# Optimization experiments

Hardware: AMD Instinct MI355X
Metric: run time of the kernel (lower is better)

The kernel has to match this reference:

```python
import jax, jax.numpy as jnp
import numpy as np

QB = 127.0  # act_bits=8 -> 2**(8-1)-1
EPS = 1e-5


def _ste(x, q):
    # straight-through estimator: forward = q, backward = identity
    return x + jax.lax.stop_gradient(q - x)


def bitlinear(x, W, b):
    """BitNet-b1.58 linear: ternary weights (per-tensor mean-abs scale),
    8-bit per-token absmax activations, dequantized matmul + bias."""
    w_scale = jnp.clip(jnp.mean(jnp.abs(W)), EPS, None)
    Wq = _ste(W, jnp.clip(jnp.round(W / w_scale), -1.0, 1.0) * w_scale)  # ternary * scale
    x_scale = jnp.clip(jnp.max(jnp.abs(x), axis=-1, keepdims=True), EPS, None)
    xq = _ste(x, jnp.clip(jnp.round(x * (QB / x_scale)), -QB - 1.0, QB) * (x_scale / QB))
    # x: [B, N, d_in], W: [d_out, d_in] -> [B, N, d_out]
    return jnp.einsum('bnd,hd->bnh', xq, Wq) + b


def setup_inputs() -> dict:
    key = jax.random.key(0)
    k0, k1, k2 = jax.random.split(key, 3)
    B, N, D = 8, 4096, 1024
    H = int(D * 4.0)
    x = jax.random.normal(k0, (B, N, D), dtype=jnp.float32)
    W1 = jax.random.normal(k1, (H, D), dtype=jnp.float32) * 0.02
    b1 = jnp.zeros((H,), dtype=jnp.float32)
    W2 = jax.random.normal(k2, (D, H), dtype=jnp.float32) * 0.02
    b2 = jnp.zeros((D,), dtype=jnp.float32)
    return {"x": x, "W1": W1, "b1": b1, "W2": W2, "b2": b2}


def reference(x, W1, b1, W2, b2):
    h = bitlinear(x, W1, b1)                 # [B, N, H]
    h = jax.nn.gelu(h, approximate=False)    # torch nn.GELU default = exact erf
    # dropout with p=0.0 is identity
    return bitlinear(h, W2, b2)              # [B, N, D]
```

## Files before the change

kernel.cpp:

```cpp
#include <hip/hip_runtime.h>
#include <hip/hip_bf16.h>
#include <math.h>


typedef int int32x4 __attribute__((ext_vector_type(4)));

typedef const void __attribute__((address_space(1))) gv_t;
typedef void __attribute__((address_space(3))) lv_t;

__device__ __forceinline__ void gload_lds16(const signed char* g,
                                            signed char* l) {
  __builtin_amdgcn_global_load_lds((gv_t*)g, (lv_t*)l, 16, 0, 0);
}

__device__ __forceinline__ float gelu_erf(float v) {
  return 0.5f * v * (1.0f + erff(v * 0.70710678118654752440f));
}

__device__ __forceinline__ void store_gt(float* p, float v) { *p = v; }
__device__ __forceinline__ void store_gt(__hip_bfloat16* p, float v) {
  unsigned u = __float_as_uint(v);
  u += 0x7fffu + ((u >> 16) & 1u);
  *(unsigned short*)p = (unsigned short)(u >> 16);
}

__device__ __forceinline__ void load4v(const float* p, float v[4]) {
  const float4 t = *(const float4*)p;
  v[0] = t.x; v[1] = t.y; v[2] = t.z; v[3] = t.w;
}
__device__ __forceinline__ void load4v(const __hip_bfloat16* p, float v[4]) {
  const ushort4 t = *(const ushort4*)p;
  v[0] = __uint_as_float((unsigned)t.x << 16);
  v[1] = __uint_as_float((unsigned)t.y << 16);
  v[2] = __uint_as_float((unsigned)t.z << 16);
  v[3] = __uint_as_float((unsigned)t.w << 16);
}

__global__ __launch_bounds__(256) void absmean_partial(
    const float* __restrict__ W, double* __restrict__ part) {
  const int tid = threadIdx.x;
  const long base = (long)blockIdx.x * 8192;
  double s = 0.0;
#pragma unroll
  for (int c = 0; c < 8; ++c) {
    const float4 v = *(const float4*)&W[base + c * 1024 + tid * 4];
    s += (double)fabsf(v.x) + (double)fabsf(v.y) +
         (double)fabsf(v.z) + (double)fabsf(v.w);
  }
  __shared__ double sm[256];
  sm[tid] = s; __syncthreads();
  for (int off = 128; off; off >>= 1) {
    if (tid < off) sm[tid] += sm[tid + off];
    __syncthreads();
  }
  if (tid == 0) part[blockIdx.x] = sm[0];
}

__global__ __launch_bounds__(256) void absmean_final(
    const double* __restrict__ part, double* __restrict__ out, double n) {
  const int tid = threadIdx.x;
  __shared__ double sm[256];
  sm[tid] = part[tid] + part[tid + 256];
  __syncthreads();
  for (int off = 128; off; off >>= 1) {
    if (tid < off) sm[tid] += sm[tid + off];
    __syncthreads();
  }
  if (tid == 0) out[0] = fmax(sm[0] / n, 1e-5);
}

__global__ __launch_bounds__(256) void quant_w(
    const float* __restrict__ W, const double* __restrict__ wsP,
    signed char* __restrict__ Wq) {
  const double ws = *wsP;
  const long i = ((long)blockIdx.x * 256 + threadIdx.x) * 4;
  const float4 v = *(const float4*)&W[i];
  const float vv[4] = {v.x, v.y, v.z, v.w};
  int pack = 0;
#pragma unroll
  for (int q = 0; q < 4; ++q) {
    double r = rint((double)vv[q] / ws);
    r = fmin(fmax(r, -1.0), 1.0);
    pack |= (((int)r) & 0xff) << (8 * q);
  }
  *(int*)&Wq[i] = pack;
}

template <int L, bool GELU, typename GT>
__global__ __launch_bounds__(256) void quant_rows(
    const GT* __restrict__ X, signed char* __restrict__ Xq,
    float* __restrict__ dsc) {
  constexpr int CH = L / 1024;
  const long row = blockIdx.x;
  const int tid = threadIdx.x;
  const GT* xr = X + row * (long)L;
  float v[CH][4];
  float m = 0.f;
#pragma unroll
  for (int c = 0; c < CH; ++c) {
    load4v(xr + c * 1024 + tid * 4, v[c]);
#pragma unroll
    for (int q = 0; q < 4; ++q) {
      if (GELU) v[c][q] = gelu_erf(v[c][q]);
      m = fmaxf(m, fabsf(v[c][q]));
    }
  }
#pragma unroll
  for (int off = 32; off; off >>= 1) m = fmaxf(m, __shfl_down(m, off, 64));
  __shared__ float wmx[4];
  if ((tid & 63) == 0) wmx[tid >> 6] = m;
  __syncthreads();
  float ms = fmaxf(fmaxf(wmx[0], wmx[1]), fmaxf(wmx[2], wmx[3]));
  ms = fmaxf(ms, 1e-5f);
  const double inv = 127.0 / (double)ms;
#pragma unroll
  for (int c = 0; c < CH; ++c) {
    int pack = 0;
#pragma unroll
    for (int q = 0; q < 4; ++q) {
      double r = rint((double)v[c][q] * inv);
      r = fmin(fmax(r, -128.0), 127.0);
      pack |= (((int)r) & 0xff) << (8 * q);
    }
    *(int*)&Xq[row * (long)L + c * 1024 + tid * 4] = pack;
  }
  if (tid == 0) dsc[row] = (float)((double)ms / 127.0);
}

template <typename GT>
__global__ __launch_bounds__(256, 2) void gemm_i8_occ(
    const signed char* __restrict__ A, const signed char* __restrict__ Bm,
    const float* __restrict__ dA, const double* __restrict__ wsB,
    const float* __restrict__ bias, GT* __restrict__ C,
    int K, int Ncol, int nx) {
  __shared__ signed char LDS[65536];
  const int tid = threadIdx.x;
  const int lane = tid & 63;
  const int wave = tid >> 6;
  const int wm = wave >> 1;
  const int wn = wave & 1;

  const int cpx = gridDim.x >> 3;
  const int wg = ((int)blockIdx.x & 7) * cpx + ((int)blockIdx.x >> 3);
  const long rowBase = (long)(wg / nx) * 128;
  const long colBase = (long)(wg % nx) * 128;
  const int NT = K >> 7;

  const int dd = tid << 4;
  const int srow = dd >> 7;
  const int scol = (dd & 127) ^ ((srow & 7) << 4);
  const long k32 = 32L * K;
  const signed char* sA0 = A + (rowBase + srow) * (long)K + scol;
  const signed char* sB0 = Bm + (colBase + srow) * (long)K + scol;

  auto STAGE = [&](int t) {
    const signed char* pa = sA0 + ((long)t << 7);
    const signed char* pb = sB0 + ((long)t << 7);
    signed char* la = &LDS[((t & 1) << 14) + dd];
    signed char* lb = &LDS[32768 + ((t & 1) << 14) + dd];
#pragma unroll
    for (int i = 0; i < 4; ++i) gload_lds16(pa + i * k32, la + i * 4096);
#pragma unroll
    for (int i = 0; i < 4; ++i) gload_lds16(pb + i * k32, lb + i * 4096);
  };

  const int rl = lane & 15;
  const int col0 = (((lane >> 4) << 4)) ^ ((rl & 7) << 4);
  const int aRow = wm * 8192 + rl * 128;
  const int bRow = wn * 8192 + rl * 128;

  int32x4 acc[4][4] = {};
  int32x4 af0[4], bf0[4], af1[4], bf1[4];

  STAGE(0);

  for (int t = 0; t < NT; ++t) {
    const signed char* At = &LDS[(t & 1) << 14];
    const signed char* Bt = &LDS[32768 + ((t & 1) << 14)];

    if (t + 1 < NT) {
      STAGE(t + 1);
      asm volatile("s_waitcnt vmcnt(8)" ::: "memory");
    } else {
      asm volatile("s_waitcnt vmcnt(0)" ::: "memory");
    }
    __builtin_amdgcn_s_barrier();

#pragma unroll
    for (int i = 0; i < 4; ++i)
      af0[i] = *(const int32x4*)(At + aRow + i * 2048 + col0);
#pragma unroll
    for (int j = 0; j < 4; ++j)
      bf0[j] = *(const int32x4*)(Bt + bRow + j * 2048 + col0);
#pragma unroll
    for (int i = 0; i < 4; ++i)
      af1[i] = *(const int32x4*)(At + aRow + i * 2048 + (col0 ^ 64));
#pragma unroll
    for (int j = 0; j < 4; ++j)
      bf1[j] = *(const int32x4*)(Bt + bRow + j * 2048 + (col0 ^ 64));

    __builtin_amdgcn_s_setprio(1);
#pragma unroll
    for (int i = 0; i < 4; ++i)
#pragma unroll
      for (int j = 0; j < 4; ++j)
        acc[i][j] = __builtin_amdgcn_mfma_i32_16x16x64_i8(
            af0[i], bf0[j], acc[i][j], 0, 0, 0);
#pragma unroll
    for (int i = 0; i < 4; ++i)
#pragma unroll
      for (int j = 0; j < 4; ++j)
        acc[i][j] = __builtin_amdgcn_mfma_i32_16x16x64_i8(
            af1[i], bf1[j], acc[i][j], 0, 0, 0);
    __builtin_amdgcn_s_setprio(0);

    asm volatile("s_waitcnt lgkmcnt(0)" ::: "memory");
    __builtin_amdgcn_s_barrier();
  }

  const double wsd = *wsB;
  const int rq = (lane >> 4) << 2;
  float bv[4];
#pragma unroll
  for (int nj = 0; nj < 4; ++nj)
    bv[nj] = bias[colBase + wn * 64 + nj * 16 + rl];
#pragma unroll
  for (int mi = 0; mi < 4; ++mi) {
#pragma unroll
    for (int r = 0; r < 4; ++r) {
      const long row = rowBase + wm * 64 + mi * 16 + rq + r;
      const float sc = (float)((double)dA[row] * wsd);
      GT* crow = C + row * (long)Ncol + colBase + wn * 64 + rl;
#pragma unroll
      for (int nj = 0; nj < 4; ++nj)
        store_gt(&crow[nj * 16], (float)acc[mi][nj][r] * sc + bv[nj]);
    }
  }
}

extern "C" void kernel_launch(void* const* d_in, const int* in_sizes, int n_in,
                              void* d_out, int out_size, void* d_ws,
                              size_t ws_size, hipStream_t stream) {
  const float* x  = (const float*)d_in[0];
  const float* W1 = (const float*)d_in[1];
  const float* b1 = (const float*)d_in[2];
  const float* W2 = (const float*)d_in[3];
  const float* b2 = (const float*)d_in[4];
  const int D = in_sizes[4];
  const int H = in_sizes[2];
  const long M = (long)in_sizes[0] / D;
  float* out = (float*)d_out;

  if (D != 1024 || H != 4096 || (M % 128) != 0) return;

  char* wsp = (char*)d_ws;
  size_t off = 0;
  auto alloc = [&](size_t bytes) {
    void* p = wsp + off;
    off = (off + bytes + 255) & ~(size_t)255;
    return p;
  };
  signed char* wq1 = (signed char*)alloc((size_t)H * D);
  signed char* wq2 = (signed char*)alloc((size_t)D * H);
  signed char* xq  = (signed char*)alloc((size_t)M * D);
  signed char* gq  = (signed char*)alloc((size_t)M * H);
  float* dx = (float*)alloc((size_t)M * 4);
  float* dg = (float*)alloc((size_t)M * 4);
  double* part = (double*)alloc(512 * 8);
  double* ws1 = (double*)alloc(8);
  double* ws2 = (double*)alloc(8);
  __hip_bfloat16* h = (__hip_bfloat16*)alloc((size_t)M * H * 2);
  if (off > ws_size) return;

  const long nW = (long)H * D;
  absmean_partial<<<nW / 8192, 256, 0, stream>>>(W1, part);
  absmean_final<<<1, 256, 0, stream>>>(part, ws1, (double)nW);
  absmean_partial<<<nW / 8192, 256, 0, stream>>>(W2, part);
  absmean_final<<<1, 256, 0, stream>>>(part, ws2, (double)nW);
  quant_w<<<nW / 1024, 256, 0, stream>>>(W1, ws1, wq1);
  quant_w<<<nW / 1024, 256, 0, stream>>>(W2, ws2, wq2);
  quant_rows<1024, false, float><<<M, 256, 0, stream>>>(x, xq, dx);

  const int g1 = (int)(M / 128) * (H / 128);
  const int g2 = (int)(M / 128) * (D / 128);
  gemm_i8_occ<__hip_bfloat16><<<g1, 256, 0, stream>>>(
      xq, wq1, dx, ws1, b1, h, D, H, H / 128);
  quant_rows<4096, true, __hip_bfloat16><<<M, 256, 0, stream>>>(h, gq, dg);
  gemm_i8_occ<float><<<g2, 256, 0, stream>>>(
      gq, wq2, dg, ws2, b2, out, H, D, D / 128);
}
```

Before: 516.4 us.

## Widen int8 GEMM tile to 128x256 with 8 waves and BK=64

Rewrites the int8 MFMA GEMM to use 512-thread blocks with 8 waves in a 2x4 arrangement, each block computing a 128x256 output tile instead of 128x128. The K step per stage drops from 128 to 64, LDS shrinks to 48KB, and the XOR swizzle is adapted to 64-byte rows. The goal is more reuse of the A tile per block and higher occupancy (launch bounds 512,4). In exchange there are more K iterations, each with its own barrier, and fewer blocks in the grid, particularly for the second GEMM.

```diff
diff --git a/kernel.cpp b/kernel.cpp
--- a/kernel.cpp
+++ b/kernel.cpp
@@ -128,90 +128,73 @@
 }
 
 template <typename GT>
-__global__ __launch_bounds__(256, 2) void gemm_i8_occ(
+__global__ __launch_bounds__(512, 4) void gemm_i8_2b(
     const signed char* __restrict__ A, const signed char* __restrict__ Bm,
     const float* __restrict__ dA, const double* __restrict__ wsB,
     const float* __restrict__ bias, GT* __restrict__ C,
     int K, int Ncol, int nx) {
-  __shared__ signed char LDS[65536];
+  __shared__ signed char LDS[49152];
   const int tid = threadIdx.x;
   const int lane = tid & 63;
   const int wave = tid >> 6;
-  const int wm = wave >> 1;
-  const int wn = wave & 1;
+  const int wm = wave >> 2;
+  const int wn = wave & 3;
 
   const int cpx = gridDim.x >> 3;
   const int wg = ((int)blockIdx.x & 7) * cpx + ((int)blockIdx.x >> 3);
   const long rowBase = (long)(wg / nx) * 128;
-  const long colBase = (long)(wg % nx) * 128;
-  const int NT = K >> 7;
-
-  const int dd = tid << 4;
-  const int srow = dd >> 7;
-  const int scol = (dd & 127) ^ ((srow & 7) << 4);
-  const long k32 = 32L * K;
-  const signed char* sA0 = A + (rowBase + srow) * (long)K + scol;
-  const signed char* sB0 = Bm + (colBase + srow) * (long)K + scol;
+  const long colBase = (long)(wg % nx) * 256;
+  const int NT = K >> 6;
+
+  const int sr = tid >> 2;
+  const int sc = ((tid & 3) << 4) ^ ((sr & 3) << 4);
+  const signed char* gAr = A + (rowBase + sr) * (long)K + sc;
+  const signed char* gBr = Bm + (colBase + sr) * (long)K + sc;
+  const signed char* gBr2 = gBr + 128L * K;
+  const int da = tid << 4;
 
   auto STAGE = [&](int t) {
-    const signed char* pa = sA0 + ((long)t << 7);
-    const signed char* pb = sB0 + ((long)t << 7);
-    signed char* la = &LDS[((t & 1) << 14) + dd];
-    signed char* lb = &LDS[32768 + ((t & 1) << 14) + dd];
-#pragma unroll
-    for (int i = 0; i < 4; ++i) gload_lds16(pa + i * k32, la + i * 4096);
-#pragma unroll
-    for (int i = 0; i < 4; ++i) gload_lds16(pb + i * k32, lb + i * 4096);
+    const long ko = (long)t << 6;
+    gload_lds16(gAr + ko, &LDS[((t & 1) << 13) + da]);
+    gload_lds16(gBr + ko, &LDS[16384 + ((t & 1) << 14) + da]);
+    gload_lds16(gBr2 + ko, &LDS[16384 + ((t & 1) << 14) + 8192 + da]);
   };
 
   const int rl = lane & 15;
-  const int col0 = (((lane >> 4) << 4)) ^ ((rl & 7) << 4);
-  const int aRow = wm * 8192 + rl * 128;
-  const int bRow = wn * 8192 + rl * 128;
+  const int axor = (((lane >> 4) ^ (rl & 3)) << 4);
+  const int aoff = (wm * 64 + rl) * 64 + axor;
+  const int boff = (wn * 64 + rl) * 64 + axor;
 
   int32x4 acc[4][4] = {};
-  int32x4 af0[4], bf0[4], af1[4], bf1[4];
+  int32x4 af[4], bf[4];
 
   STAGE(0);
 
   for (int t = 0; t < NT; ++t) {
-    const signed char* At = &LDS[(t & 1) << 14];
-    const signed char* Bt = &LDS[32768 + ((t & 1) << 14)];
-
     if (t + 1 < NT) {
       STAGE(t + 1);
-      asm volatile("s_waitcnt vmcnt(8)" ::: "memory");
+      asm volatile("s_waitcnt vmcnt(3)" ::: "memory");
     } else {
       asm volatile("s_waitcnt vmcnt(0)" ::: "memory");
     }
     __builtin_amdgcn_s_barrier();
 
-#pragma unroll
-    for (int i = 0; i < 4; ++i)
-      af0[i] = *(const int32x4*)(At + aRow + i * 2048 + col0);
-#pragma unroll
-    for (int j = 0; j < 4; ++j)
-      bf0[j] = *(const int32x4*)(Bt + bRow + j * 2048 + col0);
-#pragma unroll
-    for (int i = 0; i < 4; ++i)
-      af1[i] = *(const int32x4*)(At + aRow + i * 2048 + (col0 ^ 64));
-#pragma unroll
-    for (int j = 0; j < 4; ++j)
-      bf1[j] = *(const int32x4*)(Bt + bRow + j * 2048 + (col0 ^ 64));
+    const signed char* At = &LDS[(t & 1) << 13];
+    const signed char* Bt = &LDS[16384 + ((t & 1) << 14)];
+#pragma unroll
+    for (int mi = 0; mi < 4; ++mi)
+      af[mi] = *(const int32x4*)(At + aoff + mi * 1024);
+#pragma unroll
+    for (int nj = 0; nj < 4; ++nj)
+      bf[nj] = *(const int32x4*)(Bt + boff + nj * 1024);
 
     __builtin_amdgcn_s_setprio(1);
 #pragma unroll
-    for (int i = 0; i < 4; ++i)
-#pragma unroll
-      for (int j = 0; j < 4; ++j)
-        acc[i][j] = __builtin_amdgcn_mfma_i32_16x16x64_i8(
-            af0[i], bf0[j], acc[i][j], 0, 0, 0);
-#pragma unroll
-    for (int i = 0; i < 4; ++i)
-#pragma unroll
-      for (int j = 0; j < 4; ++j)
-        acc[i][j] = __builtin_amdgcn_mfma_i32_16x16x64_i8(
-            af1[i], bf1[j], acc[i][j], 0, 0, 0);
+    for (int mi = 0; mi < 4; ++mi)
+#pragma unroll
+      for (int nj = 0; nj < 4; ++nj)
+        acc[mi][nj] = __builtin_amdgcn_mfma_i32_16x16x64_i8(
+            af[mi], bf[nj], acc[mi][nj], 0, 0, 0);
     __builtin_amdgcn_s_setprio(0);
 
     asm volatile("s_waitcnt lgkmcnt(0)" ::: "memory");
@@ -229,11 +212,11 @@
 #pragma unroll
     for (int r = 0; r < 4; ++r) {
       const long row = rowBase + wm * 64 + mi * 16 + rq + r;
-      const float sc = (float)((double)dA[row] * wsd);
+      const float sc2 = (float)((double)dA[row] * wsd);
       GT* crow = C + row * (long)Ncol + colBase + wn * 64 + rl;
 #pragma unroll
       for (int nj = 0; nj < 4; ++nj)
-        store_gt(&crow[nj * 16], (float)acc[mi][nj][r] * sc + bv[nj]);
+        store_gt(&crow[nj * 16], (float)acc[mi][nj][r] * sc2 + bv[nj]);
     }
   }
 }
@@ -281,11 +264,11 @@
   quant_w<<<nW / 1024, 256, 0, stream>>>(W2, ws2, wq2);
   quant_rows<1024, false, float><<<M, 256, 0, stream>>>(x, xq, dx);
 
-  const int g1 = (int)(M / 128) * (H / 128);
-  const int g2 = (int)(M / 128) * (D / 128);
-  gemm_i8_occ<__hip_bfloat16><<<g1, 256, 0, stream>>>(
-      xq, wq1, dx, ws1, b1, h, D, H, H / 128);
+  const int g1 = (int)(M / 128) * (H / 256);
+  const int g2 = (int)(M / 128) * (D / 256);
+  gemm_i8_2b<__hip_bfloat16><<<g1, 512, 0, stream>>>(
+      xq, wq1, dx, ws1, b1, h, D, H, H / 256);
   quant_rows<4096, true, __hip_bfloat16><<<M, 256, 0, stream>>>(h, gq, dg);
-  gemm_i8_occ<float><<<g2, 256, 0, stream>>>(
-      gq, wq2, dg, ws2, b2, out, H, D, D / 128);
-}
+  gemm_i8_2b<float><<<g2, 512, 0, stream>>>(
+      gq, wq2, dg, ws2, b2, out, H, D, D / 256);
+}
```

After: 499.1 us. 3.4% less time.
